# Kernel optimization log

Hardware: AMD Instinct MI355X
Metric: run time of the kernel (lower is better)

## Reference

```python
import jax, jax.numpy as jnp
import numpy as np

B, S, D = 4, 256, 768
DEP = 100
H, DK = 12, 64


def setup_inputs() -> dict:
    key = jax.random.key(0)
    ks = jax.random.split(key, 6)
    std_v = float(np.sqrt(2.0 / (D + D)))
    std_e = float(np.sqrt(2.0 / (DEP + DK)))
    return {
        "token_feature": jax.random.normal(ks[0], (B, S, D), dtype=jnp.float32),
        "edge_feature": jax.random.normal(ks[1], (B, S, S, DEP), dtype=jnp.float32),
        "dependency_masks": jax.random.randint(ks[2], (B, S, S), 0, 2, dtype=jnp.int32),
        "W_v": jax.random.normal(ks[3], (D, D), dtype=jnp.float32) * std_v,
        "W_e": jax.random.normal(ks[4], (DEP, D), dtype=jnp.float32) * std_e,
        "w_rel": jax.random.normal(ks[5], (DK,), dtype=jnp.float32) * (1.0 / np.sqrt(DK)),
    }


def reference(token_feature, edge_feature, dependency_masks, W_v, W_e, w_rel):
    b, s, d = token_feature.shape
    dk = w_rel.shape[0]
    h = d // dk
    # value projection per token j: [b, j, h, dk] (no need to replicate over i)
    V = (token_feature @ W_v).reshape(b, s, h, dk)
    # edge value per (i, j) pair: [b, i, j, h, dk]
    Ev = (edge_feature @ W_e).reshape(b, s, s, h, dk)
    # scalar score per (head, i, j): relu(Linear(dk -> 1))
    scores = jax.nn.relu(jnp.einsum("bijhd,d->bhij", Ev, w_rel))
    # mask: positions with dependency_masks == 0 get -1e6 (pre-softmax)
    scores = jnp.where(dependency_masks[:, None, :, :] == 0, jnp.float32(-1e6), scores)
    probs = jax.nn.softmax(scores, axis=-1)  # [b, h, i, j]; dropout = identity (eval)
    # weighted sum over neighbors j -> [b, i, h, dk] -> [b, s, d]
    ctx = jnp.einsum("bhij,bjhd->bihd", probs, V).reshape(b, s, d)
    return jax.nn.relu(token_feature + ctx)
```

## Files before the change

### kernel.cpp

```cpp
#include <hip/hip_runtime.h>
#include <math.h>

#define BB 4
#define SS 256
#define DD 768
#define DEPC 100
#define HH 12

typedef short bf16x8 __attribute__((ext_vector_type(8)));
typedef float f32x4 __attribute__((ext_vector_type(4)));

__device__ __forceinline__ unsigned short f2bf(float x) {
    unsigned int u = __float_as_uint(x);
    u += 0x7FFF + ((u >> 16) & 1);
    return (unsigned short)(u >> 16);
}
__device__ __forceinline__ float bf2f(unsigned short h) {
    return __uint_as_float(((unsigned int)h) << 16);
}

__global__ __launch_bounds__(256) void k_prep(const float* __restrict__ W_e,
                                              const float* __restrict__ w_rel,
                                              const float* __restrict__ W_v,
                                              unsigned short* __restrict__ upk,
                                              unsigned short* __restrict__ wpk) {
    int t = threadIdx.x;
    if (blockIdx.x == 0) {
        __shared__ float u_l[HH][DEPC];
        const float4* wr = (const float4*)w_rel;
        float4 wrv[16];
#pragma unroll
        for (int c = 0; c < 16; ++c) wrv[c] = wr[c];
        for (int e = t; e < DEPC * HH; e += 256) {
            int p = e / HH, h = e % HH;
            const float4* we = (const float4*)(W_e + p * DD + h * 64);
            float acc = 0.f;
#pragma unroll
            for (int c = 0; c < 16; ++c) {
                float4 a = we[c], b = wrv[c];
                acc += a.x * b.x + a.y * b.y + a.z * b.z + a.w * b.w;
            }
            u_l[h][p] = acc;
        }
        __syncthreads();
        int s = t >> 6, l = t & 63;
        int h = l & 15, kg = l >> 4;
        unsigned short hi[8], lo[8];
#pragma unroll
        for (int e = 0; e < 8; ++e) {
            int k = 32 * s + kg * 8 + e;
            float v = (h < HH && k < DEPC) ? u_l[h][k] : 0.f;
            unsigned short hb = f2bf(v);
            hi[e] = hb;
            lo[e] = f2bf(v - bf2f(hb));
        }
        unsigned short* dh = upk + (s * 64 + l) * 8;
        unsigned short* dl = upk + 2048 + (s * 64 + l) * 8;
#pragma unroll
        for (int e = 0; e < 8; ++e) { dh[e] = hi[e]; dl[e] = lo[e]; }
    } else {
        int unit = (blockIdx.x - 1) * 4 + (t >> 6);
        int lane = t & 63;
        int s = unit / 48, ct = unit % 48;
        int cl = lane & 15, kg = lane >> 4;
        unsigned short hi[8], lo[8];
#pragma unroll
        for (int e = 0; e < 8; ++e) {
            int k = s * 32 + kg * 8 + e;
            float v = W_v[(size_t)k * DD + ct * 16 + cl];
            unsigned short hb = f2bf(v);
            hi[e] = hb;
            lo[e] = f2bf(v - bf2f(hb));
        }
        size_t base = ((size_t)(s * 48 + ct) * 64 + lane) * 8;
        unsigned short* dh = wpk + base;
        unsigned short* dl = wpk + 589824 + base;
#pragma unroll
        for (int e = 0; e < 8; ++e) { dh[e] = hi[e]; dl[e] = lo[e]; }
    }
}

__device__ __forceinline__ void body_v(char* smem, int unit, int t,
                                       const float* __restrict__ A,
                                       const unsigned short* __restrict__ wpk,
                                       unsigned short* __restrict__ Vbf) {
    unsigned short* Ah = (unsigned short*)smem;
    unsigned short* Al = Ah + 2560;
#define AH(bf, r, c) Ah[((bf) * 32 + (r)) * 40 + (c)]
#define AL(bf, r, c) Al[((bf) * 32 + (r)) * 40 + (c)]
    int lane = t & 63, w = t >> 6;
    int wr = w >> 1, wc = w & 1;
    int vr = unit & 31, c0y = unit >> 5;
    int r0 = vr * 32;
    int srow = t >> 3, sq = t & 7;

    {
        float4 av = *(const float4*)&A[(size_t)(r0 + srow) * DD + 4 * sq];
        const float* af = (const float*)&av;
#pragma unroll
        for (int e = 0; e < 4; ++e) {
            unsigned short hb = f2bf(af[e]);
            AH(0, srow, 4 * sq + e) = hb;
            AL(0, srow, 4 * sq + e) = f2bf(af[e] - bf2f(hb));
        }
    }
    __syncthreads();

    int ct = c0y * 2 + wc;
    int fr = wr * 16 + (lane & 15);
    int kg = lane >> 4;
    f32x4 acc = {0.f, 0.f, 0.f, 0.f};

    for (int s = 0; s < 24; ++s) {
        float4 nx = {0, 0, 0, 0};
        if (s + 1 < 24)
            nx = *(const float4*)&A[(size_t)(r0 + srow) * DD + (s + 1) * 32 + 4 * sq];

        const unsigned short* bp = wpk + ((size_t)(s * 48 + ct) * 64 + lane) * 8;
        bf16x8 bh = *(const bf16x8*)bp;
        bf16x8 bl = *(const bf16x8*)(bp + 589824);
        bf16x8 ah = *(const bf16x8*)&AH(s & 1, fr, kg * 8);
        bf16x8 al = *(const bf16x8*)&AL(s & 1, fr, kg * 8);
        acc = __builtin_amdgcn_mfma_f32_16x16x32_bf16(ah, bh, acc, 0, 0, 0);
        acc = __builtin_amdgcn_mfma_f32_16x16x32_bf16(al, bh, acc, 0, 0, 0);
        acc = __builtin_amdgcn_mfma_f32_16x16x32_bf16(ah, bl, acc, 0, 0, 0);

        if (s + 1 < 24) {
            const float* nf = (const float*)&nx;
            int nb = (s + 1) & 1;
#pragma unroll
            for (int e = 0; e < 4; ++e) {
                unsigned short hb = f2bf(nf[e]);
                AH(nb, srow, 4 * sq + e) = hb;
                AL(nb, srow, 4 * sq + e) = f2bf(nf[e] - bf2f(hb));
            }
        }
        __syncthreads();
    }

    int col = c0y * 32 + wc * 16 + (lane & 15);
    int rowb = r0 + wr * 16 + (lane >> 4) * 4;
#pragma unroll
    for (int e = 0; e < 4; ++e)
        Vbf[(size_t)(rowb + e) * DD + col] = f2bf(acc[e]);
#undef AH
#undef AL
}

__device__ __forceinline__ void body_sc(int jc, int i, int b, int t,
                                        const float* __restrict__ edge,
                                        const int* __restrict__ mask,
                                        const unsigned short* __restrict__ upk,
                                        float* __restrict__ scores) {
    int lane = t & 63, w = t >> 6;
    int arow = lane & 15, kg = lane >> 4;
    int j0 = jc * 64 + w * 16;
    const float* rbase = edge + (size_t)((b * SS + i) * SS + j0 + arow) * DEPC + kg * 8;

    float4 va[4], vb[4];
#pragma unroll
    for (int s = 0; s < 3; ++s) {
        va[s] = *(const float4*)(rbase + 32 * s);
        vb[s] = *(const float4*)(rbase + 32 * s + 4);
    }
    va[3] = (kg == 0) ? *(const float4*)(rbase + 96)
                      : make_float4(0.f, 0.f, 0.f, 0.f);
    vb[3] = make_float4(0.f, 0.f, 0.f, 0.f);

    bf16x8 uh[4], ul[4];
#pragma unroll
    for (int s = 0; s < 4; ++s) {
        uh[s] = *(const bf16x8*)(upk + (s * 64 + lane) * 8);
        ul[s] = *(const bf16x8*)(upk + 2048 + (s * 64 + lane) * 8);
    }

    int4 mk = *(const int4*)(mask + (size_t)(b * SS + i) * SS + j0 + kg * 4);

    f32x4 acc = {0.f, 0.f, 0.f, 0.f};
#pragma unroll
    for (int s = 0; s < 4; ++s) {
        float ev[8] = {va[s].x, va[s].y, va[s].z, va[s].w,
                       vb[s].x, vb[s].y, vb[s].z, vb[s].w};
        bf16x8 ehi, elo;
#pragma unroll
        for (int e = 0; e < 8; ++e) {
            unsigned short hb = f2bf(ev[e]);
            ehi[e] = (short)hb;
            elo[e] = (short)f2bf(ev[e] - bf2f(hb));
        }
        acc = __builtin_amdgcn_mfma_f32_16x16x32_bf16(ehi, uh[s], acc, 0, 0, 0);
        acc = __builtin_amdgcn_mfma_f32_16x16x32_bf16(ehi, ul[s], acc, 0, 0, 0);
        acc = __builtin_amdgcn_mfma_f32_16x16x32_bf16(elo, uh[s], acc, 0, 0, 0);
    }

    int h = lane & 15;
    int js = j0 + kg * 4;
    float4 r;
    r.x = mk.x ? fmaxf(acc[0], 0.f) : -1e6f;
    r.y = mk.y ? fmaxf(acc[1], 0.f) : -1e6f;
    r.z = mk.z ? fmaxf(acc[2], 0.f) : -1e6f;
    r.w = mk.w ? fmaxf(acc[3], 0.f) : -1e6f;
    if (h < HH)
        *(float4*)&scores[(((size_t)b * HH + h) * SS + i) * SS + js] = r;
}

__global__ __launch_bounds__(256) void k_main(const float* __restrict__ token,
                                              const unsigned short* __restrict__ wpk,
                                              unsigned short* __restrict__ Vbf,
                                              const float* __restrict__ edge,
                                              const int* __restrict__ mask,
                                              const unsigned short* __restrict__ upk,
                                              float* __restrict__ scores) {
    __shared__ __align__(16) char smem[10240];
    int t = threadIdx.x;
    int x = blockIdx.x, b = blockIdx.y;
    if (x < 192) {
        int unit = b * 192 + x;
        body_v(smem, unit, t, token, wpk, Vbf);
    } else {
        int xx = x - 192;
        body_sc(xx & 3, xx >> 2, b, t, edge, mask, upk, scores);
    }
}

__global__ __launch_bounds__(256) void k_ctx(const float* __restrict__ scores,
                                             const unsigned short* __restrict__ Vbf,
                                             const float* __restrict__ token,
                                             float* __restrict__ out) {
    __shared__ float P[16][260];
    __shared__ unsigned short Pb[16][264];
    int t = threadIdx.x;
    int i0 = blockIdx.x * 16, h = blockIdx.y, b = blockIdx.z;
    int lane = t & 63, w = t >> 6;

    const float* sbase = scores + (((size_t)b * HH + h) * SS + i0) * SS;
#pragma unroll
    for (int k = 0; k < 4; ++k) {
        int idx = t + 256 * k;
        int r = idx >> 6, jc = idx & 63;
        float4 v = *(const float4*)(sbase + (size_t)r * SS + 4 * jc);
        *(float4*)&P[r][4 * jc] = v;
    }
    __syncthreads();

    for (int r = w; r < 16; r += 4) {
        float x0 = P[r][lane],       x1 = P[r][lane + 64];
        float x2 = P[r][lane + 128], x3 = P[r][lane + 192];
        float m = fmaxf(fmaxf(x0, x1), fmaxf(x2, x3));
#pragma unroll
        for (int o = 32; o > 0; o >>= 1) m = fmaxf(m, __shfl_xor(m, o, 64));
        x0 = __expf(x0 - m); x1 = __expf(x1 - m);
        x2 = __expf(x2 - m); x3 = __expf(x3 - m);
        float s = x0 + x1 + x2 + x3;
#pragma unroll
        for (int o = 32; o > 0; o >>= 1) s += __shfl_xor(s, o, 64);
        float inv = 1.0f / s;
        Pb[r][lane]       = f2bf(x0 * inv);
        Pb[r][lane + 64]  = f2bf(x1 * inv);
        Pb[r][lane + 128] = f2bf(x2 * inv);
        Pb[r][lane + 192] = f2bf(x3 * inv);
    }
    __syncthreads();

    int cl = lane & 15, kg = lane >> 4;
    f32x4 acc = {0.f, 0.f, 0.f, 0.f};
    const unsigned short* vb = Vbf + (size_t)b * SS * DD + h * 64 + w * 16 + cl;
#pragma unroll
    for (int s = 0; s < 8; ++s) {
        bf16x8 af = *(const bf16x8*)&Pb[cl][s * 32 + kg * 8];
        bf16x8 bfr;
#pragma unroll
        for (int e = 0; e < 8; ++e)
            bfr[e] = (short)vb[(size_t)(s * 32 + kg * 8 + e) * DD];
        acc = __builtin_amdgcn_mfma_f32_16x16x32_bf16(af, bfr, acc, 0, 0, 0);
    }

    int col = h * 64 + w * 16 + cl;
#pragma unroll
    for (int e = 0; e < 4; ++e) {
        size_t o = (size_t)(b * SS + i0 + kg * 4 + e) * DD + col;
        out[o] = fmaxf(token[o] + acc[e], 0.f);
    }
}

extern "C" void kernel_launch(void* const* d_in, const int* in_sizes, int n_in,
                              void* d_out, int out_size, void* d_ws, size_t ws_size,
                              hipStream_t stream) {
    const float* token = (const float*)d_in[0];
    const float* edge  = (const float*)d_in[1];
    const int*   mask  = (const int*)d_in[2];
    const float* W_v   = (const float*)d_in[3];
    const float* W_e   = (const float*)d_in[4];
    const float* w_rel = (const float*)d_in[5];
    float* out = (float*)d_out;

    char* ws = (char*)d_ws;
    unsigned short* upk = (unsigned short*)(ws);
    unsigned short* wpk = (unsigned short*)(ws + 8192);
    unsigned short* Vbf = (unsigned short*)(ws + 8192 + 2359296);
    float* scores = (float*)(ws + 8192 + 2359296 + 1572864 + 1024);

    hipLaunchKernelGGL(k_prep, dim3(289),              dim3(256), 0, stream, W_e, w_rel, W_v, upk, wpk);
    hipLaunchKernelGGL(k_main, dim3(192 + SS * 4, BB), dim3(256), 0, stream,
                       token, wpk, Vbf, edge, mask, upk, scores);
    hipLaunchKernelGGL(k_ctx,  dim3(16, HH, BB),       dim3(256), 0, stream, scores, Vbf, token, out);
}
```

Before: 54.89 us.

## Fuse softmax into score kernel and pass bf16 probabilities to context kernel

Each score block now handles a full query row (all 256 keys) instead of a quarter, stages the masked scores in shared memory, computes the softmax in place, and writes bf16 probabilities to global memory. The context kernel then reads those bf16 probabilities directly, with no fp32 score staging or softmax of its own. This halves the intermediate traffic and removes a shared-memory pass from the context kernel. In exchange there are four times fewer score blocks, each doing more serial work, plus a block-wide barrier and more shared memory per block, which may reduce occupancy.

```diff
diff --git a/kernel.cpp b/kernel.cpp
--- a/kernel.cpp
+++ b/kernel.cpp
@@ -147,25 +147,14 @@
 #undef AL
 }
 
-__device__ __forceinline__ void body_sc(int jc, int i, int b, int t,
+__device__ __forceinline__ void body_sc(char* smem, int i, int b, int t,
                                         const float* __restrict__ edge,
                                         const int* __restrict__ mask,
                                         const unsigned short* __restrict__ upk,
-                                        float* __restrict__ scores) {
+                                        unsigned short* __restrict__ Pbg) {
+    float (*sc)[260] = (float(*)[260])smem;
     int lane = t & 63, w = t >> 6;
     int arow = lane & 15, kg = lane >> 4;
-    int j0 = jc * 64 + w * 16;
-    const float* rbase = edge + (size_t)((b * SS + i) * SS + j0 + arow) * DEPC + kg * 8;
-
-    float4 va[4], vb[4];
-#pragma unroll
-    for (int s = 0; s < 3; ++s) {
-        va[s] = *(const float4*)(rbase + 32 * s);
-        vb[s] = *(const float4*)(rbase + 32 * s + 4);
-    }
-    va[3] = (kg == 0) ? *(const float4*)(rbase + 96)
-                      : make_float4(0.f, 0.f, 0.f, 0.f);
-    vb[3] = make_float4(0.f, 0.f, 0.f, 0.f);
 
     bf16x8 uh[4], ul[4];
 #pragma unroll
@@ -174,34 +163,69 @@
         ul[s] = *(const bf16x8*)(upk + 2048 + (s * 64 + lane) * 8);
     }
 
-    int4 mk = *(const int4*)(mask + (size_t)(b * SS + i) * SS + j0 + kg * 4);
-
-    f32x4 acc = {0.f, 0.f, 0.f, 0.f};
-#pragma unroll
-    for (int s = 0; s < 4; ++s) {
-        float ev[8] = {va[s].x, va[s].y, va[s].z, va[s].w,
-                       vb[s].x, vb[s].y, vb[s].z, vb[s].w};
-        bf16x8 ehi, elo;
-#pragma unroll
-        for (int e = 0; e < 8; ++e) {
-            unsigned short hb = f2bf(ev[e]);
-            ehi[e] = (short)hb;
-            elo[e] = (short)f2bf(ev[e] - bf2f(hb));
-        }
-        acc = __builtin_amdgcn_mfma_f32_16x16x32_bf16(ehi, uh[s], acc, 0, 0, 0);
-        acc = __builtin_amdgcn_mfma_f32_16x16x32_bf16(ehi, ul[s], acc, 0, 0, 0);
-        acc = __builtin_amdgcn_mfma_f32_16x16x32_bf16(elo, uh[s], acc, 0, 0, 0);
-    }
-
-    int h = lane & 15;
-    int js = j0 + kg * 4;
-    float4 r;
-    r.x = mk.x ? fmaxf(acc[0], 0.f) : -1e6f;
-    r.y = mk.y ? fmaxf(acc[1], 0.f) : -1e6f;
-    r.z = mk.z ? fmaxf(acc[2], 0.f) : -1e6f;
-    r.w = mk.w ? fmaxf(acc[3], 0.f) : -1e6f;
-    if (h < HH)
-        *(float4*)&scores[(((size_t)b * HH + h) * SS + i) * SS + js] = r;
+#pragma unroll
+    for (int c = 0; c < 4; ++c) {
+        int j0 = (w * 4 + c) * 16;
+        const float* rbase = edge + (size_t)((b * SS + i) * SS + j0 + arow) * DEPC + kg * 8;
+        float4 va[4], vb[4];
+#pragma unroll
+        for (int s = 0; s < 3; ++s) {
+            va[s] = *(const float4*)(rbase + 32 * s);
+            vb[s] = *(const float4*)(rbase + 32 * s + 4);
+        }
+        va[3] = (kg == 0) ? *(const float4*)(rbase + 96)
+                          : make_float4(0.f, 0.f, 0.f, 0.f);
+        vb[3] = make_float4(0.f, 0.f, 0.f, 0.f);
+
+        int4 mk = *(const int4*)(mask + (size_t)(b * SS + i) * SS + j0 + kg * 4);
+
+        f32x4 acc = {0.f, 0.f, 0.f, 0.f};
+#pragma unroll
+        for (int s = 0; s < 4; ++s) {
+            float ev[8] = {va[s].x, va[s].y, va[s].z, va[s].w,
+                           vb[s].x, vb[s].y, vb[s].z, vb[s].w};
+            bf16x8 ehi, elo;
+#pragma unroll
+            for (int e = 0; e < 8; ++e) {
+                unsigned short hb = f2bf(ev[e]);
+                ehi[e] = (short)hb;
+                elo[e] = (short)f2bf(ev[e] - bf2f(hb));
+            }
+            acc = __builtin_amdgcn_mfma_f32_16x16x32_bf16(ehi, uh[s], acc, 0, 0, 0);
+            acc = __builtin_amdgcn_mfma_f32_16x16x32_bf16(ehi, ul[s], acc, 0, 0, 0);
+            acc = __builtin_amdgcn_mfma_f32_16x16x32_bf16(elo, uh[s], acc, 0, 0, 0);
+        }
+
+        int h = lane & 15;
+        if (h < HH) {
+            int jj = j0 + kg * 4;
+            sc[h][jj]     = mk.x ? fmaxf(acc[0], 0.f) : -1e6f;
+            sc[h][jj + 1] = mk.y ? fmaxf(acc[1], 0.f) : -1e6f;
+            sc[h][jj + 2] = mk.z ? fmaxf(acc[2], 0.f) : -1e6f;
+            sc[h][jj + 3] = mk.w ? fmaxf(acc[3], 0.f) : -1e6f;
+        }
+    }
+    __syncthreads();
+
+#pragma unroll
+    for (int r = w * 3; r < w * 3 + 3; ++r) {
+        float x0 = sc[r][lane],       x1 = sc[r][lane + 64];
+        float x2 = sc[r][lane + 128], x3 = sc[r][lane + 192];
+        float m = fmaxf(fmaxf(x0, x1), fmaxf(x2, x3));
+#pragma unroll
+        for (int o = 32; o > 0; o >>= 1) m = fmaxf(m, __shfl_xor(m, o, 64));
+        x0 = __expf(x0 - m); x1 = __expf(x1 - m);
+        x2 = __expf(x2 - m); x3 = __expf(x3 - m);
+        float s = x0 + x1 + x2 + x3;
+#pragma unroll
+        for (int o = 32; o > 0; o >>= 1) s += __shfl_xor(s, o, 64);
+        float inv = 1.0f / s;
+        unsigned short* pb = Pbg + (((size_t)(b * HH + r) * SS + i) * SS);
+        pb[lane]       = f2bf(x0 * inv);
+        pb[lane + 64]  = f2bf(x1 * inv);
+        pb[lane + 128] = f2bf(x2 * inv);
+        pb[lane + 192] = f2bf(x3 * inv);
+    }
 }
 
 __global__ __launch_bounds__(256) void k_main(const float* __restrict__ token,
@@ -210,64 +234,34 @@
                                               const float* __restrict__ edge,
                                               const int* __restrict__ mask,
                                               const unsigned short* __restrict__ upk,
-                                              float* __restrict__ scores) {
-    __shared__ __align__(16) char smem[10240];
+                                              unsigned short* __restrict__ Pbg) {
+    __shared__ __align__(16) char smem[12480];
     int t = threadIdx.x;
     int x = blockIdx.x, b = blockIdx.y;
     if (x < 192) {
         int unit = b * 192 + x;
         body_v(smem, unit, t, token, wpk, Vbf);
     } else {
-        int xx = x - 192;
-        body_sc(xx & 3, xx >> 2, b, t, edge, mask, upk, scores);
-    }
-}
-
-__global__ __launch_bounds__(256) void k_ctx(const float* __restrict__ scores,
-                                             const unsigned short* __restrict__ Vbf,
-                                             const float* __restrict__ token,
-                                             float* __restrict__ out) {
-    __shared__ float P[16][260];
-    __shared__ unsigned short Pb[16][264];
+        body_sc(smem, x - 192, b, t, edge, mask, upk, Pbg);
+    }
+}
+
+__global__ __launch_bounds__(256) void k_ctx2(const unsigned short* __restrict__ Pbg,
+                                              const unsigned short* __restrict__ Vbf,
+                                              const float* __restrict__ token,
+                                              float* __restrict__ out) {
     int t = threadIdx.x;
     int i0 = blockIdx.x * 16, h = blockIdx.y, b = blockIdx.z;
     int lane = t & 63, w = t >> 6;
-
-    const float* sbase = scores + (((size_t)b * HH + h) * SS + i0) * SS;
-#pragma unroll
-    for (int k = 0; k < 4; ++k) {
-        int idx = t + 256 * k;
-        int r = idx >> 6, jc = idx & 63;
-        float4 v = *(const float4*)(sbase + (size_t)r * SS + 4 * jc);
-        *(float4*)&P[r][4 * jc] = v;
-    }
-    __syncthreads();
-
-    for (int r = w; r < 16; r += 4) {
-        float x0 = P[r][lane],       x1 = P[r][lane + 64];
-        float x2 = P[r][lane + 128], x3 = P[r][lane + 192];
-        float m = fmaxf(fmaxf(x0, x1), fmaxf(x2, x3));
-#pragma unroll
-        for (int o = 32; o > 0; o >>= 1) m = fmaxf(m, __shfl_xor(m, o, 64));
-        x0 = __expf(x0 - m); x1 = __expf(x1 - m);
-        x2 = __expf(x2 - m); x3 = __expf(x3 - m);
-        float s = x0 + x1 + x2 + x3;
-#pragma unroll
-        for (int o = 32; o > 0; o >>= 1) s += __shfl_xor(s, o, 64);
-        float inv = 1.0f / s;
-        Pb[r][lane]       = f2bf(x0 * inv);
-        Pb[r][lane + 64]  = f2bf(x1 * inv);
-        Pb[r][lane + 128] = f2bf(x2 * inv);
-        Pb[r][lane + 192] = f2bf(x3 * inv);
-    }
-    __syncthreads();
-
-    int cl = lane & 15, kg = lane >> 4;
+    int arow = lane & 15, kg = lane >> 4;
+
+    const unsigned short* prow = Pbg + ((size_t)(b * HH + h) * SS + i0 + arow) * SS;
+    const unsigned short* vb = Vbf + (size_t)b * SS * DD + h * 64 + w * 16 + arow;
+
     f32x4 acc = {0.f, 0.f, 0.f, 0.f};
-    const unsigned short* vb = Vbf + (size_t)b * SS * DD + h * 64 + w * 16 + cl;
 #pragma unroll
     for (int s = 0; s < 8; ++s) {
-        bf16x8 af = *(const bf16x8*)&Pb[cl][s * 32 + kg * 8];
+        bf16x8 af = *(const bf16x8*)(prow + s * 32 + kg * 8);
         bf16x8 bfr;
 #pragma unroll
         for (int e = 0; e < 8; ++e)
@@ -275,7 +269,7 @@
         acc = __builtin_amdgcn_mfma_f32_16x16x32_bf16(af, bfr, acc, 0, 0, 0);
     }
 
-    int col = h * 64 + w * 16 + cl;
+    int col = h * 64 + w * 16 + arow;
 #pragma unroll
     for (int e = 0; e < 4; ++e) {
         size_t o = (size_t)(b * SS + i0 + kg * 4 + e) * DD + col;
@@ -298,10 +292,10 @@
     unsigned short* upk = (unsigned short*)(ws);
     unsigned short* wpk = (unsigned short*)(ws + 8192);
     unsigned short* Vbf = (unsigned short*)(ws + 8192 + 2359296);
-    float* scores = (float*)(ws + 8192 + 2359296 + 1572864 + 1024);
-
-    hipLaunchKernelGGL(k_prep, dim3(289),              dim3(256), 0, stream, W_e, w_rel, W_v, upk, wpk);
-    hipLaunchKernelGGL(k_main, dim3(192 + SS * 4, BB), dim3(256), 0, stream,
-                       token, wpk, Vbf, edge, mask, upk, scores);
-    hipLaunchKernelGGL(k_ctx,  dim3(16, HH, BB),       dim3(256), 0, stream, scores, Vbf, token, out);
-}
+    unsigned short* Pbg = (unsigned short*)(ws + 8192 + 2359296 + 1572864);
+
+    hipLaunchKernelGGL(k_prep, dim3(289),           dim3(256), 0, stream, W_e, w_rel, W_v, upk, wpk);
+    hipLaunchKernelGGL(k_main, dim3(192 + SS, BB),  dim3(256), 0, stream,
+                       token, wpk, Vbf, edge, mask, upk, Pbg);
+    hipLaunchKernelGGL(k_ctx2, dim3(16, HH, BB),    dim3(256), 0, stream, Pbg, Vbf, token, out);
+}
```

After: 52.41 us (median of 2 runs). -4.5%, faster.
